# Performance work log

Hardware: AMD Instinct MI355X
Metric: run time of the kernel (lower is better)

## Reference

```python
import jax, jax.numpy as jnp
import numpy as np
from jax.scipy.linalg import expm

BINS = 100
LO, HI = -5.0, 5.0
ENT_THRESH = 2.5
EPS = 1e-9


def _batched_histc(x):
    # torch.histc(sample, bins=100, min=-5, max=5): out-of-range values ignored,
    # x == HI lands in the last bin.
    B = x.shape[0]
    width = (HI - LO) / BINS
    idx = jnp.clip(jnp.floor((x - LO) / width).astype(jnp.int32), 0, BINS - 1)
    in_range = ((x >= LO) & (x <= HI)).astype(x.dtype)
    flat_idx = (idx + BINS * jnp.arange(B, dtype=jnp.int32)[:, None]).ravel()
    hist = jax.ops.segment_sum(in_range.ravel(), flat_idx, num_segments=B * BINS)
    return hist.reshape(B, BINS)


def _policy(s, w1, b1, w2, b2):
    return jax.nn.relu(s @ w1 + b1) @ w2 + b2


def setup_inputs() -> dict:
    key = jax.random.key(0)
    ks = jax.random.split(key, 5)
    B, D, N, A, H = 16384, 5120, 512, 64, 128
    return {
        "event_stream": jax.random.normal(ks[0], (B, D), jnp.float32),
        "sensing_matrix": jax.random.normal(ks[1], (N, D), jnp.float32),
        "adjacency": jax.random.normal(ks[2], (N, N), jnp.float32) * 0.05,
        "w1": jax.random.normal(ks[3], (N, H), jnp.float32) / np.float32(np.sqrt(N)),
        "b1": jnp.zeros((H,), jnp.float32),
        "w2": jax.random.normal(ks[4], (H, A), jnp.float32) / np.float32(np.sqrt(H)),
        "b2": jnp.zeros((A,), jnp.float32),
    }


def reference(event_stream, sensing_matrix, adjacency, w1, b1, w2, b2):
    # Layer 1: batched histogram + Shannon-entropy gate (replaces per-sample loop)
    hist = _batched_histc(event_stream)                       # [B, 100]
    p = hist / (hist.sum(-1, keepdims=True) + EPS)
    h = -(p * jnp.log(p + EPS)).sum(-1)                       # [B]
    passed = h >= ENT_THRESH                                   # low entropy -> zeroed row
    compressed = event_stream @ sensing_matrix.T               # [B, N]
    filtered = jnp.where(passed[:, None], compressed, jnp.zeros((), event_stream.dtype))
    # Layer 2: NOTEARS acyclicity constraint + causal state
    n = adjacency.shape[0]
    h_acyclic = jnp.trace(expm(adjacency * adjacency)) - jnp.asarray(n, adjacency.dtype)
    state = filtered @ adjacency                               # [B, N]
    # Layer 3: robust (FGSM-style) policy, training branch of the original
    g = jax.grad(lambda s: _policy(s, w1, b1, w2, b2).mean())(state)
    robust_logits = _policy(state - 0.1 * jnp.sign(g), w1, b1, w2, b2)
    action_probs = jax.nn.softmax(robust_logits, axis=-1)      # [B, A]
    return (action_probs, h_acyclic)
```

## Files before the change

kernel.cpp:

```cpp
#include <hip/hip_runtime.h>

typedef unsigned short u16;
typedef short s16x8 __attribute__((ext_vector_type(8)));
typedef float f32x4 __attribute__((ext_vector_type(4)));
typedef u16   u16x4 __attribute__((ext_vector_type(4)));

#define GLDS16(g, l) __builtin_amdgcn_global_load_lds( \
    (const __attribute__((address_space(1))) void*)(g), \
    (__attribute__((address_space(3))) void*)(l), 16, 0, 0)

__device__ __forceinline__ void split1(float x, u16& h, u16& l) {
  __bf16 hb = (__bf16)x;
  __bf16 lb = (__bf16)(x - (float)hb);
  h = __builtin_bit_cast(u16, hb);
  l = __builtin_bit_cast(u16, lb);
}

__global__ __launch_bounds__(256) void k_hist(const float* __restrict__ E,
                                              float* __restrict__ flags) {
  __shared__ unsigned int hist[100];
  const int tid = threadIdx.x;
  const int row = blockIdx.x;
  if (tid < 100) hist[tid] = 0u;
  __syncthreads();
  const float4* rp = (const float4*)(E + (size_t)row * 5120);
#pragma unroll
  for (int j = 0; j < 5; ++j) {
    float4 v = rp[j * 256 + tid];
    float xs[4] = {v.x, v.y, v.z, v.w};
#pragma unroll
    for (int c = 0; c < 4; ++c) {
      float x = xs[c];
      float t = (x + 5.0f) / 0.1f;
      int b = (int)floorf(t);
      b = b < 0 ? 0 : (b > 99 ? 99 : b);
      if (x >= -5.0f && x <= 5.0f) atomicAdd(&hist[b], 1u);
    }
  }
  __syncthreads();
  if (tid == 0) {
    float S = 0.f;
    for (int i = 0; i < 100; ++i) S += (float)hist[i];
    float d = S + 1e-9f;
    float h = 0.f;
    for (int i = 0; i < 100; ++i) {
      float p = (float)hist[i] / d;
      h -= p * logf(p + 1e-9f);
    }
    flags[row] = (h >= 2.5f) ? 1.0f : 0.0f;
  }
}

__global__ void k_convert(const float* __restrict__ X, u16* __restrict__ Xh,
                          u16* __restrict__ Xl, int n4) {
  int idx = blockIdx.x * 256 + threadIdx.x;
  if (idx < n4) {
    float4 v = ((const float4*)X)[idx];
    u16 h0, h1, h2, h3, l0, l1, l2, l3;
    split1(v.x, h0, l0); split1(v.y, h1, l1);
    split1(v.z, h2, l2); split1(v.w, h3, l3);
    ((u16x4*)Xh)[idx] = u16x4{h0, h1, h2, h3};
    ((u16x4*)Xl)[idx] = u16x4{l0, l1, l2, l3};
  }
}

__global__ void k_prep_adj(const float* __restrict__ adj, u16* __restrict__ aTh,
                           u16* __restrict__ aTl, float* __restrict__ Mf,
                           u16* __restrict__ Mth, u16* __restrict__ Mtl) {
  int idx = blockIdx.x * 256 + threadIdx.x;
  if (idx >= 512 * 512) return;
  int i = idx >> 9, j = idx & 511;
  float a = adj[idx];
  float m = a * a;
  Mf[idx] = m;
  u16 h, l;
  split1(a, h, l); aTh[j * 512 + i] = h; aTl[j * 512 + i] = l;
  split1(m, h, l); Mth[j * 512 + i] = h; Mtl[j * 512 + i] = l;
}

__global__ void k_prep_w1t(const float* __restrict__ w1, float* __restrict__ w1T) {
  int idx = blockIdx.x * 256 + threadIdx.x;
  if (idx < 512 * 128) { int n = idx >> 7, h = idx & 127; w1T[h * 512 + n] = w1[idx]; }
}

__global__ __launch_bounds__(256, 2) void gemm_sbf16(
    const float* __restrict__ A, const u16* __restrict__ Bh,
    const u16* __restrict__ Bl, float* __restrict__ C,
    const float* __restrict__ flags, int N, int K) {
  __shared__ u16 lAh[128 * 64], lAl[128 * 64], lBh[128 * 64], lBl[128 * 64];
  const int tid = threadIdx.x;
  const int lane = tid & 63;
  const int w = tid >> 6;
  const int wm = (w >> 1) * 64, wn = (w & 1) * 64;
  const int row0 = blockIdx.y * 128;
  const int col0 = blockIdx.x * 128;

  f32x4 acc[4][4] = {};

  const int rr = lane & 15;
  const int kgrp = (lane >> 4) * 8;
  const int sw = (rr & 7) << 3;
  const int bsrc = (((lane & 7) ^ (lane >> 3)) << 3);
  const int brow = lane >> 3;

  const int nk = K >> 6;
  for (int kt = 0; kt < nk; ++kt) {
    const int k0 = kt << 6;
    {
      const int rbase = w * 32;
#pragma unroll
      for (int i = 0; i < 4; ++i) {
        const size_t gro = (size_t)(col0 + rbase + i * 8 + brow) * K + k0 + bsrc;
        GLDS16(Bh + gro, &lBh[(rbase + i * 8) * 64]);
        GLDS16(Bl + gro, &lBl[(rbase + i * 8) * 64]);
      }
    }
    float4 av[8];
#pragma unroll
    for (int j = 0; j < 8; ++j) {
      int idx = j * 256 + tid;
      int r = idx >> 4, kv = (idx & 15) * 4;
      av[j] = *(const float4*)(A + (size_t)(row0 + r) * K + k0 + kv);
    }
#pragma unroll
    for (int j = 0; j < 8; ++j) {
      int idx = j * 256 + tid;
      int r = idx >> 4, kv = (idx & 15) * 4;
      int col = kv ^ ((r & 7) << 3);
      u16 h0, h1, h2, h3, l0, l1, l2, l3;
      split1(av[j].x, h0, l0); split1(av[j].y, h1, l1);
      split1(av[j].z, h2, l2); split1(av[j].w, h3, l3);
      *(u16x4*)&lAh[r * 64 + col] = u16x4{h0, h1, h2, h3};
      *(u16x4*)&lAl[r * 64 + col] = u16x4{l0, l1, l2, l3};
    }
    __syncthreads();
#pragma unroll
    for (int kk = 0; kk < 2; ++kk) {
      const int kx = (kk * 32 + kgrp) ^ sw;
      s16x8 ah[4], al[4], bh[4], bl[4];
#pragma unroll
      for (int mi = 0; mi < 4; ++mi) {
        const int r = (wm + mi * 16 + rr) * 64 + kx;
        ah[mi] = *(const s16x8*)&lAh[r];
        al[mi] = *(const s16x8*)&lAl[r];
      }
#pragma unroll
      for (int ni = 0; ni < 4; ++ni) {
        const int r = (wn + ni * 16 + rr) * 64 + kx;
        bh[ni] = *(const s16x8*)&lBh[r];
        bl[ni] = *(const s16x8*)&lBl[r];
      }
#pragma unroll
      for (int mi = 0; mi < 4; ++mi)
#pragma unroll
        for (int ni = 0; ni < 4; ++ni) {
          acc[mi][ni] = __builtin_amdgcn_mfma_f32_16x16x32_bf16(ah[mi], bh[ni], acc[mi][ni], 0, 0, 0);
          acc[mi][ni] = __builtin_amdgcn_mfma_f32_16x16x32_bf16(ah[mi], bl[ni], acc[mi][ni], 0, 0, 0);
          acc[mi][ni] = __builtin_amdgcn_mfma_f32_16x16x32_bf16(al[mi], bh[ni], acc[mi][ni], 0, 0, 0);
        }
    }
    __syncthreads();
  }
  const int cr = (lane >> 4) * 4;
  const int cc = lane & 15;
#pragma unroll
  for (int mi = 0; mi < 4; ++mi)
#pragma unroll
    for (int j = 0; j < 4; ++j) {
      const int grow = row0 + wm + mi * 16 + cr + j;
      const float f = flags ? flags[grow] : 1.0f;
#pragma unroll
      for (int ni = 0; ni < 4; ++ni)
        C[(size_t)grow * N + col0 + wn + ni * 16 + cc] = acc[mi][ni][j] * f;
    }
}

__global__ void k_trace_diag(const float* __restrict__ M, const float* __restrict__ P2,
                             const float* __restrict__ P3, const float* __restrict__ P4,
                             const float* __restrict__ P5, const float* __restrict__ P6,
                             float* __restrict__ tr) {
  __shared__ float red[8];
  const float* mats[6] = {M, P2, P3, P4, P5, P6};
  const int t = threadIdx.x;
  if (t < 6) tr[6 + t] = 0.0f;
  for (int s = 0; s < 6; ++s) {
    float v = mats[s][t * 513];
#pragma unroll
    for (int off = 32; off; off >>= 1) v += __shfl_down(v, off);
    if ((t & 63) == 0) red[t >> 6] = v;
    __syncthreads();
    if (t == 0) {
      float a = 0.f;
      for (int i = 0; i < 8; ++i) a += red[i];
      tr[s] = a;
    }
    __syncthreads();
  }
}

__global__ void k_trace_dot(const float* __restrict__ Pa, const float* __restrict__ Pb,
                            float* __restrict__ slot) {
  int idx = blockIdx.x * 256 + threadIdx.x;
  float acc = 0.f;
  for (int t = idx; t < 512 * 512; t += 65536) {
    int i = t >> 9, j = t & 511;
    acc += Pa[t] * Pb[(j << 9) + i];
  }
#pragma unroll
  for (int off = 32; off; off >>= 1) acc += __shfl_down(acc, off);
  if ((threadIdx.x & 63) == 0) atomicAdd(slot, acc);
}

__global__ void k_finalize(const float* __restrict__ tr, float* __restrict__ outh) {
  if (threadIdx.x == 0) {
    double h = 0.0, f = 1.0;
    for (int k = 1; k <= 12; ++k) { f *= k; h += (double)tr[k - 1] / f; }
    outh[0] = (float)h;
  }
}

__global__ __launch_bounds__(256, 2) void k_policy(
    const float* __restrict__ state, const float* __restrict__ w1,
    const float* __restrict__ w1T, const float* __restrict__ w2,
    const float* __restrict__ b1, const float* __restrict__ b2,
    float* __restrict__ out) {
  __shared__ float s[16][513];
  __shared__ float q[16][130];
  __shared__ float Rp[16][130];
  __shared__ float lg[16][66];
  __shared__ float csum[128];
  const int tid = threadIdx.x;
  const int r0 = blockIdx.x * 16;

#pragma unroll
  for (int j = 0; j < 8; ++j) {
    int idx = j * 256 + tid;
    int r = idx >> 7, c4 = (idx & 127) * 4;
    float4 v = *(const float4*)(state + (size_t)(r0 + r) * 512 + c4);
    s[r][c4 + 0] = v.x; s[r][c4 + 1] = v.y; s[r][c4 + 2] = v.z; s[r][c4 + 3] = v.w;
  }
  if (tid < 128) {
    float a = 0.f;
    const float4* wp = (const float4*)(w2 + tid * 64);
#pragma unroll
    for (int i = 0; i < 16; ++i) { float4 v = wp[i]; a += v.x + v.y + v.z + v.w; }
    csum[tid] = a;
  }
  __syncthreads();

  {
    const int h4 = (tid & 31) * 4;
    const int rg = (tid >> 5) * 2;
    float z00 = 0, z01 = 0, z02 = 0, z03 = 0, z10 = 0, z11 = 0, z12 = 0, z13 = 0;
#pragma unroll 4
    for (int n = 0; n < 512; ++n) {
      float4 wv = *(const float4*)(w1 + (size_t)n * 128 + h4);
      float s0 = s[rg][n], s1 = s[rg + 1][n];
      z00 += s0 * wv.x; z01 += s0 * wv.y; z02 += s0 * wv.z; z03 += s0 * wv.w;
      z10 += s1 * wv.x; z11 += s1 * wv.y; z12 += s1 * wv.z; z13 += s1 * wv.w;
    }
    float4 bb = *(const float4*)(b1 + h4);
    q[rg][h4 + 0] = (z00 + bb.x > 0.f) ? csum[h4 + 0] : 0.f;
    q[rg][h4 + 1] = (z01 + bb.y > 0.f) ? csum[h4 + 1] : 0.f;
    q[rg][h4 + 2] = (z02 + bb.z > 0.f) ? csum[h4 + 2] : 0.f;
    q[rg][h4 + 3] = (z03 + bb.w > 0.f) ? csum[h4 + 3] : 0.f;
    q[rg + 1][h4 + 0] = (z10 + bb.x > 0.f) ? csum[h4 + 0] : 0.f;
    q[rg + 1][h4 + 1] = (z11 + bb.y > 0.f) ? csum[h4 + 1] : 0.f;
    q[rg + 1][h4 + 2] = (z12 + bb.z > 0.f) ? csum[h4 + 2] : 0.f;
    q[rg + 1][h4 + 3] = (z13 + bb.w > 0.f) ? csum[h4 + 3] : 0.f;
  }
  __syncthreads();

  {
    const int n4 = (tid & 127) * 4;
    const int rg = (tid >> 7) * 8;
    float g[8][4] = {};
#pragma unroll 2
    for (int h = 0; h < 128; ++h) {
      float4 wv = *(const float4*)(w1T + (size_t)h * 512 + n4);
#pragma unroll
      for (int i = 0; i < 8; ++i) {
        float qq = q[rg + i][h];
        g[i][0] += qq * wv.x; g[i][1] += qq * wv.y;
        g[i][2] += qq * wv.z; g[i][3] += qq * wv.w;
      }
    }
#pragma unroll
    for (int i = 0; i < 8; ++i)
#pragma unroll
      for (int c = 0; c < 4; ++c) {
        float gg = g[i][c];
        float sgn = (gg > 0.f) ? 1.f : ((gg < 0.f) ? -1.f : 0.f);
        s[rg + i][n4 + c] -= 0.1f * sgn;
      }
  }
  __syncthreads();

  {
    const int h4 = (tid & 31) * 4;
    const int rg = (tid >> 5) * 2;
    float z00 = 0, z01 = 0, z02 = 0, z03 = 0, z10 = 0, z11 = 0, z12 = 0, z13 = 0;
#pragma unroll 4
    for (int n = 0; n < 512; ++n) {
      float4 wv = *(const float4*)(w1 + (size_t)n * 128 + h4);
      float s0 = s[rg][n], s1 = s[rg + 1][n];
      z00 += s0 * wv.x; z01 += s0 * wv.y; z02 += s0 * wv.z; z03 += s0 * wv.w;
      z10 += s1 * wv.x; z11 += s1 * wv.y; z12 += s1 * wv.z; z13 += s1 * wv.w;
    }
    float4 bb = *(const float4*)(b1 + h4);
    Rp[rg][h4 + 0] = fmaxf(z00 + bb.x, 0.f);
    Rp[rg][h4 + 1] = fmaxf(z01 + bb.y, 0.f);
    Rp[rg][h4 + 2] = fmaxf(z02 + bb.z, 0.f);
    Rp[rg][h4 + 3] = fmaxf(z03 + bb.w, 0.f);
    Rp[rg + 1][h4 + 0] = fmaxf(z10 + bb.x, 0.f);
    Rp[rg + 1][h4 + 1] = fmaxf(z11 + bb.y, 0.f);
    Rp[rg + 1][h4 + 2] = fmaxf(z12 + bb.z, 0.f);
    Rp[rg + 1][h4 + 3] = fmaxf(z13 + bb.w, 0.f);
  }
  __syncthreads();

  {
    const int a4 = (tid & 15) * 4;
    const int r = tid >> 4;
    float L0 = 0, L1 = 0, L2 = 0, L3 = 0;
#pragma unroll 4
    for (int h = 0; h < 128; ++h) {
      float rp = Rp[r][h];
      float4 wv = *(const float4*)(w2 + (size_t)h * 64 + a4);
      L0 += rp * wv.x; L1 += rp * wv.y; L2 += rp * wv.z; L3 += rp * wv.w;
    }
    float4 bb = *(const float4*)(b2 + a4);
    lg[r][a4 + 0] = L0 + bb.x; lg[r][a4 + 1] = L1 + bb.y;
    lg[r][a4 + 2] = L2 + bb.z; lg[r][a4 + 3] = L3 + bb.w;
  }
  __syncthreads();

  if (tid < 16) {
    float mx = -3.0e38f;
    for (int a = 0; a < 64; ++a) mx = fmaxf(mx, lg[tid][a]);
    float sum = 0.f;
    for (int a = 0; a < 64; ++a) { float e = __expf(lg[tid][a] - mx); lg[tid][a] = e; sum += e; }
    float inv = 1.f / sum;
    for (int a = 0; a < 64; ++a) lg[tid][a] *= inv;
  }
  __syncthreads();
#pragma unroll
  for (int j = 0; j < 4; ++j) {
    int idx = j * 256 + tid;
    int r = idx >> 6, a = idx & 63;
    out[(size_t)(r0 + r) * 64 + a] = lg[r][a];
  }
}

extern "C" void kernel_launch(void* const* d_in, const int* in_sizes, int n_in,
                              void* d_out, int out_size, void* d_ws, size_t ws_size,
                              hipStream_t stream) {
  const float* E   = (const float*)d_in[0];
  const float* S   = (const float*)d_in[1];
  const float* adj = (const float*)d_in[2];
  const float* w1  = (const float*)d_in[3];
  const float* b1  = (const float*)d_in[4];
  const float* w2  = (const float*)d_in[5];
  const float* b2  = (const float*)d_in[6];
  float* out = (float*)d_out;

  char* wsb = (char*)d_ws;
  size_t off = 0;
  auto alloc = [&](size_t bytes) { void* p = wsb + off; off += (bytes + 255) & ~(size_t)255; return p; };
  u16*   Sh   = (u16*)alloc((size_t)512 * 5120 * 2);
  u16*   Sl   = (u16*)alloc((size_t)512 * 5120 * 2);
  float* filt = (float*)alloc((size_t)16384 * 512 * 4);
  float* st   = (float*)alloc((size_t)16384 * 512 * 4);
  float* w1T  = (float*)alloc((size_t)128 * 512 * 4);
  float* flg  = (float*)alloc((size_t)16384 * 4);
  u16*   aTh  = (u16*)alloc((size_t)512 * 512 * 2);
  u16*   aTl  = (u16*)alloc((size_t)512 * 512 * 2);
  float* Mf   = (float*)alloc((size_t)512 * 512 * 4);
  u16*   Mth  = (u16*)alloc((size_t)512 * 512 * 2);
  u16*   Mtl  = (u16*)alloc((size_t)512 * 512 * 2);
  float* P2   = (float*)alloc((size_t)512 * 512 * 4);
  float* P3   = (float*)alloc((size_t)512 * 512 * 4);
  float* P4   = (float*)alloc((size_t)512 * 512 * 4);
  float* P5   = (float*)alloc((size_t)512 * 512 * 4);
  float* P6   = (float*)alloc((size_t)512 * 512 * 4);
  float* tr   = (float*)alloc(256);
  (void)in_sizes; (void)n_in; (void)out_size; (void)ws_size;

  k_hist<<<16384, 256, 0, stream>>>(E, flg);
  k_convert<<<2560, 256, 0, stream>>>(S, Sh, Sl, 512 * 5120 / 4);
  k_prep_adj<<<1024, 256, 0, stream>>>(adj, aTh, aTl, Mf, Mth, Mtl);
  k_prep_w1t<<<256, 256, 0, stream>>>(w1, w1T);

  dim3 gBig(4, 128);
  gemm_sbf16<<<gBig, 256, 0, stream>>>(E, Sh, Sl, filt, flg, 512, 5120);
  gemm_sbf16<<<gBig, 256, 0, stream>>>(filt, aTh, aTl, st, nullptr, 512, 512);

  dim3 gSm(4, 4);
  gemm_sbf16<<<gSm, 256, 0, stream>>>(Mf, Mth, Mtl, P2, nullptr, 512, 512);
  gemm_sbf16<<<gSm, 256, 0, stream>>>(P2, Mth, Mtl, P3, nullptr, 512, 512);
  gemm_sbf16<<<gSm, 256, 0, stream>>>(P3, Mth, Mtl, P4, nullptr, 512, 512);
  gemm_sbf16<<<gSm, 256, 0, stream>>>(P4, Mth, Mtl, P5, nullptr, 512, 512);
  gemm_sbf16<<<gSm, 256, 0, stream>>>(P5, Mth, Mtl, P6, nullptr, 512, 512);

  k_trace_diag<<<1, 512, 0, stream>>>(Mf, P2, P3, P4, P5, P6, tr);
  k_trace_dot<<<256, 256, 0, stream>>>(P3, P4, tr + 6);
  k_trace_dot<<<256, 256, 0, stream>>>(P4, P4, tr + 7);
  k_trace_dot<<<256, 256, 0, stream>>>(P4, P5, tr + 8);
  k_trace_dot<<<256, 256, 0, stream>>>(P5, P5, tr + 9);
  k_trace_dot<<<256, 256, 0, stream>>>(P5, P6, tr + 10);
  k_trace_dot<<<256, 256, 0, stream>>>(P6, P6, tr + 11);
  k_finalize<<<1, 64, 0, stream>>>(tr, out + (size_t)16384 * 64);

  k_policy<<<1024, 256, 0, stream>>>(st, w1, w1T, w2, b1, b2, out);
}
```

Measured before the change: 1.188 ms.

## Fold adjacency into sensing matrix, shorten expm trace series, restructure histogram

Precomputes W = S^T·adj once, so the large GEMM writes the final state directly and the separate filtered·adj GEMM over 16384 rows goes away. The expm trace series is cut from 12 to 8 terms. Powers M3 and M4 are computed in one launch, and all traces come from a single fused reduction kernel that also finalizes through a completion counter. The histogram uses one wavefront per row with a shuffle-based entropy reduction, and the large GEMM gets a remapped block order. Reassociating the matmuls and truncating the series changes rounding and the series-truncation error in exchange for less GEMM work and fewer kernel launches.

After: 999.4 us. 15.9% less time.

```diff
diff --git a/kernel.cpp b/kernel.cpp
--- a/kernel.cpp
+++ b/kernel.cpp
@@ -18,63 +18,72 @@
 
 __global__ __launch_bounds__(256) void k_hist(const float* __restrict__ E,
                                               float* __restrict__ flags) {
-  __shared__ unsigned int hist[100];
-  const int tid = threadIdx.x;
-  const int row = blockIdx.x;
-  if (tid < 100) hist[tid] = 0u;
+  __shared__ unsigned int H4[4][104];
+  const int lane = threadIdx.x & 63;
+  const int w = threadIdx.x >> 6;
+  const int row = blockIdx.x * 4 + w;
+  unsigned int* H = H4[w];
+  for (int b = lane; b < 104; b += 64) H[b] = 0u;
   __syncthreads();
   const float4* rp = (const float4*)(E + (size_t)row * 5120);
-#pragma unroll
-  for (int j = 0; j < 5; ++j) {
-    float4 v = rp[j * 256 + tid];
+#pragma unroll 4
+  for (int j = 0; j < 20; ++j) {
+    float4 v = rp[j * 64 + lane];
     float xs[4] = {v.x, v.y, v.z, v.w};
 #pragma unroll
     for (int c = 0; c < 4; ++c) {
       float x = xs[c];
-      float t = (x + 5.0f) / 0.1f;
+      float t = (x - (-5.0f)) / 0.1f;
       int b = (int)floorf(t);
       b = b < 0 ? 0 : (b > 99 ? 99 : b);
-      if (x >= -5.0f && x <= 5.0f) atomicAdd(&hist[b], 1u);
-    }
-  }
-  __syncthreads();
-  if (tid == 0) {
-    float S = 0.f;
-    for (int i = 0; i < 100; ++i) S += (float)hist[i];
-    float d = S + 1e-9f;
-    float h = 0.f;
-    for (int i = 0; i < 100; ++i) {
-      float p = (float)hist[i] / d;
-      h -= p * logf(p + 1e-9f);
-    }
-    flags[row] = (h >= 2.5f) ? 1.0f : 0.0f;
-  }
-}
-
-__global__ void k_convert(const float* __restrict__ X, u16* __restrict__ Xh,
-                          u16* __restrict__ Xl, int n4) {
+      if (x >= -5.0f && x <= 5.0f) atomicAdd(&H[b], 1u);
+    }
+  }
+  __syncthreads();
+  float c0 = (float)H[lane];
+  float c1 = (lane < 36) ? (float)H[64 + lane] : 0.0f;
+  float tot = c0 + c1;
+#pragma unroll
+  for (int off = 32; off; off >>= 1) tot += __shfl_xor(tot, off);
+  float d = tot + 1e-9f;
+  float q0 = c0 / d, q1 = c1 / d;
+  float e = q0 * logf(q0 + 1e-9f) + q1 * logf(q1 + 1e-9f);
+#pragma unroll
+  for (int off = 32; off; off >>= 1) e += __shfl_xor(e, off);
+  if (lane == 0) flags[row] = (-e >= 2.5f) ? 1.0f : 0.0f;
+}
+
+__global__ void k_tsplit(const float* __restrict__ in, u16* __restrict__ oh,
+                         u16* __restrict__ ol, int R, int C) {
+  __shared__ float t[32][33];
+  const int c = threadIdx.x & 31, r8 = threadIdx.x >> 5;
+  const int c0 = blockIdx.x * 32, r0 = blockIdx.y * 32;
+#pragma unroll
+  for (int p = 0; p < 4; ++p)
+    t[r8 + p * 8][c] = in[(size_t)(r0 + r8 + p * 8) * C + c0 + c];
+  __syncthreads();
+#pragma unroll
+  for (int p = 0; p < 4; ++p) {
+    float v = t[c][r8 + p * 8];
+    u16 h, l; split1(v, h, l);
+    size_t o = (size_t)(c0 + r8 + p * 8) * R + r0 + c;
+    oh[o] = h; ol[o] = l;
+  }
+}
+
+__global__ void k_prep_adj(const float* __restrict__ adj, float* __restrict__ aTf,
+                           float* __restrict__ Mf, u16* __restrict__ Mth,
+                           u16* __restrict__ Mtl, float* __restrict__ tr,
+                           unsigned int* __restrict__ cnt) {
   int idx = blockIdx.x * 256 + threadIdx.x;
-  if (idx < n4) {
-    float4 v = ((const float4*)X)[idx];
-    u16 h0, h1, h2, h3, l0, l1, l2, l3;
-    split1(v.x, h0, l0); split1(v.y, h1, l1);
-    split1(v.z, h2, l2); split1(v.w, h3, l3);
-    ((u16x4*)Xh)[idx] = u16x4{h0, h1, h2, h3};
-    ((u16x4*)Xl)[idx] = u16x4{l0, l1, l2, l3};
-  }
-}
-
-__global__ void k_prep_adj(const float* __restrict__ adj, u16* __restrict__ aTh,
-                           u16* __restrict__ aTl, float* __restrict__ Mf,
-                           u16* __restrict__ Mth, u16* __restrict__ Mtl) {
-  int idx = blockIdx.x * 256 + threadIdx.x;
+  if (idx < 32) { tr[idx] = 0.0f; if (idx == 0) *cnt = 0u; }
   if (idx >= 512 * 512) return;
   int i = idx >> 9, j = idx & 511;
   float a = adj[idx];
   float m = a * a;
   Mf[idx] = m;
+  aTf[j * 512 + i] = a;
   u16 h, l;
-  split1(a, h, l); aTh[j * 512 + i] = h; aTl[j * 512 + i] = l;
   split1(m, h, l); Mth[j * 512 + i] = h; Mtl[j * 512 + i] = l;
 }
 
@@ -83,17 +92,17 @@
   if (idx < 512 * 128) { int n = idx >> 7, h = idx & 127; w1T[h * 512 + n] = w1[idx]; }
 }
 
-__global__ __launch_bounds__(256, 2) void gemm_sbf16(
+template<int EMIT>
+__device__ __forceinline__ void gemm_core(
     const float* __restrict__ A, const u16* __restrict__ Bh,
-    const u16* __restrict__ Bl, float* __restrict__ C,
-    const float* __restrict__ flags, int N, int K) {
+    const u16* __restrict__ Bl, float* __restrict__ C, u16* __restrict__ Ch,
+    u16* __restrict__ Cl, const float* __restrict__ flags, int N, int K,
+    int row0, int col0) {
   __shared__ u16 lAh[128 * 64], lAl[128 * 64], lBh[128 * 64], lBl[128 * 64];
   const int tid = threadIdx.x;
   const int lane = tid & 63;
   const int w = tid >> 6;
   const int wm = (w >> 1) * 64, wn = (w & 1) * 64;
-  const int row0 = blockIdx.y * 128;
-  const int col0 = blockIdx.x * 128;
 
   f32x4 acc[4][4] = {};
 
@@ -168,54 +177,94 @@
 #pragma unroll
     for (int j = 0; j < 4; ++j) {
       const int grow = row0 + wm + mi * 16 + cr + j;
-      const float f = flags ? flags[grow] : 1.0f;
-#pragma unroll
-      for (int ni = 0; ni < 4; ++ni)
-        C[(size_t)grow * N + col0 + wn + ni * 16 + cc] = acc[mi][ni][j] * f;
-    }
-}
-
-__global__ void k_trace_diag(const float* __restrict__ M, const float* __restrict__ P2,
-                             const float* __restrict__ P3, const float* __restrict__ P4,
-                             const float* __restrict__ P5, const float* __restrict__ P6,
-                             float* __restrict__ tr) {
-  __shared__ float red[8];
-  const float* mats[6] = {M, P2, P3, P4, P5, P6};
-  const int t = threadIdx.x;
-  if (t < 6) tr[6 + t] = 0.0f;
-  for (int s = 0; s < 6; ++s) {
-    float v = mats[s][t * 513];
-#pragma unroll
-    for (int off = 32; off; off >>= 1) v += __shfl_down(v, off);
-    if ((t & 63) == 0) red[t >> 6] = v;
-    __syncthreads();
-    if (t == 0) {
-      float a = 0.f;
-      for (int i = 0; i < 8; ++i) a += red[i];
-      tr[s] = a;
-    }
-    __syncthreads();
-  }
-}
-
-__global__ void k_trace_dot(const float* __restrict__ Pa, const float* __restrict__ Pb,
-                            float* __restrict__ slot) {
-  int idx = blockIdx.x * 256 + threadIdx.x;
-  float acc = 0.f;
-  for (int t = idx; t < 512 * 512; t += 65536) {
+      const float f = (EMIT == 0 && flags) ? flags[grow] : 1.0f;
+#pragma unroll
+      for (int ni = 0; ni < 4; ++ni) {
+        const size_t o = (size_t)grow * N + col0 + wn + ni * 16 + cc;
+        if (EMIT == 0) {
+          C[o] = acc[mi][ni][j] * f;
+        } else {
+          u16 h, l; split1(acc[mi][ni][j], h, l);
+          Ch[o] = h; Cl[o] = l;
+        }
+      }
+    }
+}
+
+template<int EMIT>
+__global__ __launch_bounds__(256, 2) void k_gemm(
+    const float* __restrict__ A, const u16* __restrict__ Bh,
+    const u16* __restrict__ Bl, float* __restrict__ C, u16* __restrict__ Ch,
+    u16* __restrict__ Cl, const float* __restrict__ flags, int N, int K) {
+  gemm_core<EMIT>(A, Bh, Bl, C, Ch, Cl, flags, N, K, blockIdx.y * 128, blockIdx.x * 128);
+}
+
+__global__ __launch_bounds__(256, 2) void k_gemm_big(
+    const float* __restrict__ A, const u16* __restrict__ Bh,
+    const u16* __restrict__ Bl, float* __restrict__ C,
+    const float* __restrict__ flags, int N, int K) {
+  int d = blockIdx.y * gridDim.x + blockIdx.x;
+  int wg = (d & 7) * 64 + (d >> 3);
+  gemm_core<0>(A, Bh, Bl, C, nullptr, nullptr, flags, N, K,
+               (wg >> 2) * 128, (wg & 3) * 128);
+}
+
+__global__ __launch_bounds__(256, 2) void k_gemm_pow(
+    const float* __restrict__ M2, const u16* __restrict__ Mth,
+    const u16* __restrict__ Mtl, const u16* __restrict__ M2th,
+    const u16* __restrict__ M2tl, float* __restrict__ M3, float* __restrict__ M4) {
+  const u16* bh = blockIdx.z ? M2th : Mth;
+  const u16* bl = blockIdx.z ? M2tl : Mtl;
+  float* c = blockIdx.z ? M4 : M3;
+  gemm_core<0>(M2, bh, bl, c, nullptr, nullptr, nullptr, 512, 512,
+               blockIdx.y * 128, blockIdx.x * 128);
+}
+
+__global__ __launch_bounds__(256) void k_traces(
+    const float* __restrict__ Mf, const float* __restrict__ M2,
+    const float* __restrict__ M3, const float* __restrict__ M4,
+    float* __restrict__ tr, unsigned int* __restrict__ cnt,
+    float* __restrict__ outh, int nblocks) {
+  float p[8] = {0.f, 0.f, 0.f, 0.f, 0.f, 0.f, 0.f, 0.f};
+  const int idx = blockIdx.x * 256 + threadIdx.x;
+  const int stride = nblocks * 256;
+  for (int t = idx; t < 512 * 512; t += stride) {
     int i = t >> 9, j = t & 511;
-    acc += Pa[t] * Pb[(j << 9) + i];
-  }
-#pragma unroll
-  for (int off = 32; off; off >>= 1) acc += __shfl_down(acc, off);
-  if ((threadIdx.x & 63) == 0) atomicAdd(slot, acc);
-}
-
-__global__ void k_finalize(const float* __restrict__ tr, float* __restrict__ outh) {
+    int tt = (j << 9) + i;
+    float a0 = Mf[t], a2 = M2[t], a3 = M3[t], a4 = M4[t];
+    float b0 = Mf[tt], b2 = M2[tt], b3 = M3[tt], b4 = M4[tt];
+    if (i == j) p[0] += a0;
+    p[1] += a0 * b0; p[2] += a0 * b2; p[3] += a2 * b2; p[4] += a2 * b3;
+    p[5] += a3 * b3; p[6] += a3 * b4; p[7] += a4 * b4;
+  }
+  const int lane = threadIdx.x & 63, w = threadIdx.x >> 6;
+#pragma unroll
+  for (int k = 0; k < 8; ++k)
+#pragma unroll
+    for (int off = 32; off; off >>= 1) p[k] += __shfl_xor(p[k], off);
+  __shared__ float red[4][8];
+  if (lane == 0)
+#pragma unroll
+    for (int k = 0; k < 8; ++k) red[w][k] = p[k];
+  __syncthreads();
+  if (threadIdx.x < 8) {
+    float s = red[0][threadIdx.x] + red[1][threadIdx.x] +
+              red[2][threadIdx.x] + red[3][threadIdx.x];
+    atomicAdd(&tr[threadIdx.x], s);
+  }
+  __threadfence();
+  __syncthreads();
   if (threadIdx.x == 0) {
-    double h = 0.0, f = 1.0;
-    for (int k = 1; k <= 12; ++k) { f *= k; h += (double)tr[k - 1] / f; }
-    outh[0] = (float)h;
+    unsigned int done = atomicAdd(cnt, 1u);
+    if (done == (unsigned int)(nblocks - 1)) {
+      double h = 0.0, f = 1.0;
+      for (int k = 1; k <= 8; ++k) {
+        f *= k;
+        float tk = atomicAdd(&tr[k - 1], 0.0f);
+        h += (double)tk / f;
+      }
+      outh[0] = (float)h;
+    }
   }
 }
 
@@ -367,49 +416,38 @@
   char* wsb = (char*)d_ws;
   size_t off = 0;
   auto alloc = [&](size_t bytes) { void* p = wsb + off; off += (bytes + 255) & ~(size_t)255; return p; };
-  u16*   Sh   = (u16*)alloc((size_t)512 * 5120 * 2);
-  u16*   Sl   = (u16*)alloc((size_t)512 * 5120 * 2);
-  float* filt = (float*)alloc((size_t)16384 * 512 * 4);
+  u16*   STh  = (u16*)alloc((size_t)5120 * 512 * 2);
+  u16*   STl  = (u16*)alloc((size_t)5120 * 512 * 2);
+  u16*   WTh  = (u16*)alloc((size_t)512 * 5120 * 2);
+  u16*   WTl  = (u16*)alloc((size_t)512 * 5120 * 2);
   float* st   = (float*)alloc((size_t)16384 * 512 * 4);
   float* w1T  = (float*)alloc((size_t)128 * 512 * 4);
   float* flg  = (float*)alloc((size_t)16384 * 4);
-  u16*   aTh  = (u16*)alloc((size_t)512 * 512 * 2);
-  u16*   aTl  = (u16*)alloc((size_t)512 * 512 * 2);
+  float* aTf  = (float*)alloc((size_t)512 * 512 * 4);
   float* Mf   = (float*)alloc((size_t)512 * 512 * 4);
   u16*   Mth  = (u16*)alloc((size_t)512 * 512 * 2);
   u16*   Mtl  = (u16*)alloc((size_t)512 * 512 * 2);
-  float* P2   = (float*)alloc((size_t)512 * 512 * 4);
-  float* P3   = (float*)alloc((size_t)512 * 512 * 4);
-  float* P4   = (float*)alloc((size_t)512 * 512 * 4);
-  float* P5   = (float*)alloc((size_t)512 * 512 * 4);
-  float* P6   = (float*)alloc((size_t)512 * 512 * 4);
-  float* tr   = (float*)alloc(256);
+  float* M2   = (float*)alloc((size_t)512 * 512 * 4);
+  float* M3   = (float*)alloc((size_t)512 * 512 * 4);
+  float* M4   = (float*)alloc((size_t)512 * 512 * 4);
+  u16*   M2th = (u16*)alloc((size_t)512 * 512 * 2);
+  u16*   M2tl = (u16*)alloc((size_t)512 * 512 * 2);
+  float* tr   = (float*)alloc(128);
+  unsigned int* cnt = (unsigned int*)alloc(128);
   (void)in_sizes; (void)n_in; (void)out_size; (void)ws_size;
 
-  k_hist<<<16384, 256, 0, stream>>>(E, flg);
-  k_convert<<<2560, 256, 0, stream>>>(S, Sh, Sl, 512 * 5120 / 4);
-  k_prep_adj<<<1024, 256, 0, stream>>>(adj, aTh, aTl, Mf, Mth, Mtl);
+  k_prep_adj<<<1024, 256, 0, stream>>>(adj, aTf, Mf, Mth, Mtl, tr, cnt);
   k_prep_w1t<<<256, 256, 0, stream>>>(w1, w1T);
-
-  dim3 gBig(4, 128);
-  gemm_sbf16<<<gBig, 256, 0, stream>>>(E, Sh, Sl, filt, flg, 512, 5120);
-  gemm_sbf16<<<gBig, 256, 0, stream>>>(filt, aTh, aTl, st, nullptr, 512, 512);
-
-  dim3 gSm(4, 4);
-  gemm_sbf16<<<gSm, 256, 0, stream>>>(Mf, Mth, Mtl, P2, nullptr, 512, 512);
-  gemm_sbf16<<<gSm, 256, 0, stream>>>(P2, Mth, Mtl, P3, nullptr, 512, 512);
-  gemm_sbf16<<<gSm, 256, 0, stream>>>(P3, Mth, Mtl, P4, nullptr, 512, 512);
-  gemm_sbf16<<<gSm, 256, 0, stream>>>(P4, Mth, Mtl, P5, nullptr, 512, 512);
-  gemm_sbf16<<<gSm, 256, 0, stream>>>(P5, Mth, Mtl, P6, nullptr, 512, 512);
-
-  k_trace_diag<<<1, 512, 0, stream>>>(Mf, P2, P3, P4, P5, P6, tr);
-  k_trace_dot<<<256, 256, 0, stream>>>(P3, P4, tr + 6);
-  k_trace_dot<<<256, 256, 0, stream>>>(P4, P4, tr + 7);
-  k_trace_dot<<<256, 256, 0, stream>>>(P4, P5, tr + 8);
-  k_trace_dot<<<256, 256, 0, stream>>>(P5, P5, tr + 9);
-  k_trace_dot<<<256, 256, 0, stream>>>(P5, P6, tr + 10);
-  k_trace_dot<<<256, 256, 0, stream>>>(P6, P6, tr + 11);
-  k_finalize<<<1, 64, 0, stream>>>(tr, out + (size_t)16384 * 64);
-
+  k_tsplit<<<dim3(160, 16), 256, 0, stream>>>(S, STh, STl, 512, 5120);
+  k_gemm<1><<<dim3(40, 4), 256, 0, stream>>>(aTf, STh, STl, nullptr, WTh, WTl,
+                                             nullptr, 5120, 512);
+  k_hist<<<4096, 256, 0, stream>>>(E, flg);
+  k_gemm_big<<<dim3(4, 128), 256, 0, stream>>>(E, WTh, WTl, st, flg, 512, 5120);
+  k_gemm<0><<<dim3(4, 4), 256, 0, stream>>>(Mf, Mth, Mtl, M2, nullptr, nullptr,
+                                            nullptr, 512, 512);
+  k_tsplit<<<dim3(16, 16), 256, 0, stream>>>(M2, M2th, M2tl, 512, 512);
+  k_gemm_pow<<<dim3(4, 4, 2), 256, 0, stream>>>(M2, Mth, Mtl, M2th, M2tl, M3, M4);
+  k_traces<<<120, 256, 0, stream>>>(Mf, M2, M3, M4, tr, cnt,
+                                    out + (size_t)16384 * 64, 120);
   k_policy<<<1024, 256, 0, stream>>>(st, w1, w1T, w2, b1, b2, out);
 }
```
